# Kernel tuning notes

Measured on AMD Instinct MI355X. Metric: run time of the kernel, lower is better.

Reference implementation:

```python
import jax, jax.numpy as jnp
import numpy as np

B, N, D, C = 64, 512, 1024, 4  # batch, num_electrodes, d_model, num_classes
H = D // 2


def setup_inputs() -> dict:
    key = jax.random.key(0)
    ks = jax.random.split(key, 16)
    s = 0.02
    return {
        "Q": jax.random.normal(ks[0], (B, N, D), jnp.float32),
        "K": jax.random.normal(ks[1], (B, N, D), jnp.float32),
        "V": jax.random.normal(ks[2], (B, N, D), jnp.float32),
        "electrode_ids": jnp.arange(N, dtype=jnp.int64 if jax.config.jax_enable_x64 else jnp.int32),
        "emb": jax.random.normal(ks[3], (N, D), jnp.float32) * s,
        "dw1": jax.random.normal(ks[4], (H, D), jnp.float32) * s,
        "db1": jnp.zeros((H,), jnp.float32),
        "dw2": jax.random.normal(ks[5], (1, H), jnp.float32) * s,
        "db2": jnp.zeros((1,), jnp.float32),
        "sw1": jax.random.normal(ks[6], (H, D), jnp.float32) * s,
        "sb1": jnp.zeros((H,), jnp.float32),
        "sw2": jax.random.normal(ks[7], (1, H), jnp.float32) * s,
        "sb2": jnp.zeros((1,), jnp.float32),
        "dopamine_scale": jnp.asarray(1.0, jnp.float32),
        "serotonin_scale": jnp.asarray(1.0, jnp.float32),
        "fc_w": jax.random.normal(ks[8], (C, N * D), jnp.float32) * s,
        "fc_b": jnp.zeros((C,), jnp.float32),
    }


def reference(Q, K, V, electrode_ids, emb, dw1, db1, dw2, db2,
              sw1, sb1, sw2, sb2, dopamine_scale, serotonin_scale, fc_w, fc_b):
    e = emb[electrode_ids]                       # [N, D]
    Q = Q + e
    K = K + e
    V = V + e
    scale = jnp.sqrt(jnp.asarray(D, jnp.float32))
    scores = jnp.einsum('bnd,bmd->bnm', Q, K) / scale          # [B, N, N]
    probs = jax.nn.softmax(scores, axis=-1)
    entropy = -jnp.sum(probs * jnp.log(probs + 1e-6), axis=-1)  # [B, N]

    # dopamine MLP on Q tokens (eval mode -> dropout is identity)
    dh = jax.nn.relu(jnp.einsum('bnd,hd->bnh', Q, dw1) + db1)
    dopamine = jax.nn.sigmoid(jnp.einsum('bnh,oh->bno', dh, dw2) + db2)[..., 0]  # [B, N]

    # serotonin MLP on entropy broadcast to D identical features:
    # Linear(entropy * ones(D)) == entropy * W1.sum(axis=1) + b1 (same math, no [B,N,D] temp)
    sh = jax.nn.relu(entropy[..., None] * jnp.sum(sw1, axis=1) + sb1)            # [B, N, H]
    serotonin = jax.nn.sigmoid(jnp.einsum('bnh,oh->bno', sh, sw2) + sb2)[..., 0]  # [B, N]

    mod = dopamine_scale * dopamine[..., None] - serotonin_scale * serotonin[..., None]
    ms = scores + mod
    mu = jnp.mean(ms, axis=-1, keepdims=True)
    sd = jnp.std(ms, axis=-1, keepdims=True, ddof=1)  # torch.std default is unbiased
    ms = (ms - mu) / (sd + 1e-6)
    probs2 = jax.nn.softmax(ms, axis=-1)
    attn_out = jnp.einsum('bnm,bmd->bnd', probs2, V)   # [B, N, D]
    flat = attn_out.reshape(attn_out.shape[0], -1)      # [B, N*D]
    return flat @ fc_w.T + fc_b                          # [B, C]
```

## Files before the change

kernel.cpp:

```cpp
#include <hip/hip_runtime.h>

#define NN 512
#define ND 1024
#define NDW 524288
#define NBATCH 64

typedef __attribute__((ext_vector_type(8))) __bf16 bf16x8;
typedef __attribute__((ext_vector_type(4))) float f32x4;
typedef unsigned short u16;
typedef unsigned int u32;

__device__ __forceinline__ u16 f2bf(float x) {
    u32 u = __float_as_uint(x);
    u = (u + 0x7fffu + ((u >> 16) & 1u)) >> 16;
    return (u16)u;
}

__device__ __forceinline__ void dma16(const u16* g, const u16* l) {
    __builtin_amdgcn_global_load_lds(
        (const __attribute__((address_space(1))) u32*)(uintptr_t)g,
        (__attribute__((address_space(3))) u32*)(u32)(uintptr_t)l,
        16, 0, 0);
}

__global__ __launch_bounds__(256)
void prep_all(const float* __restrict__ Q, const float* __restrict__ K,
              const float* __restrict__ V, const int* __restrict__ eid,
              const float* __restrict__ emb,
              u16* __restrict__ Qe, u16* __restrict__ Ke, u16* __restrict__ VT,
              float* __restrict__ out, const float* __restrict__ fcb)
{
    __shared__ u16 T[64 * 72];
    const int bb = blockIdx.x;
    const int tid = threadIdx.x;

    if (bb < 16384) {
        size_t f = ((size_t)bb * 256 + tid) * 8;
        int n = (int)((f >> 10) & (NN - 1));
        int col = (int)(f & (ND - 1));
        const float* ep = emb + (size_t)eid[n] * ND + col;
        float4 e0 = *(const float4*)ep, e1 = *(const float4*)(ep + 4);
        {
            const float* qp = Q + f;
            float4 x0 = *(const float4*)qp, x1 = *(const float4*)(qp + 4);
            union { uint4 u; u16 s[8]; } o;
            o.s[0]=f2bf(x0.x+e0.x); o.s[1]=f2bf(x0.y+e0.y); o.s[2]=f2bf(x0.z+e0.z); o.s[3]=f2bf(x0.w+e0.w);
            o.s[4]=f2bf(x1.x+e1.x); o.s[5]=f2bf(x1.y+e1.y); o.s[6]=f2bf(x1.z+e1.z); o.s[7]=f2bf(x1.w+e1.w);
            *(uint4*)(Qe + f) = o.u;
        }
        {
            const float* kp = K + f;
            float4 x0 = *(const float4*)kp, x1 = *(const float4*)(kp + 4);
            union { uint4 u; u16 s[8]; } o;
            o.s[0]=f2bf(x0.x+e0.x); o.s[1]=f2bf(x0.y+e0.y); o.s[2]=f2bf(x0.z+e0.z); o.s[3]=f2bf(x0.w+e0.w);
            o.s[4]=f2bf(x1.x+e1.x); o.s[5]=f2bf(x1.y+e1.y); o.s[6]=f2bf(x1.z+e1.z); o.s[7]=f2bf(x1.w+e1.w);
            *(uint4*)(Ke + f) = o.u;
        }
    } else if (bb < 16384 + 8192) {
        const int t = bb - 16384;
        const int n0 = (t & 7) * 64, d0 = ((t >> 3) & 15) * 64, b = t >> 7;
        {
            const int r2 = (tid & 31) * 2;
            const int cg = tid >> 5;
            const int na = n0 + r2, nb = n0 + r2 + 1;
            const float* vp0 = V + ((size_t)b * NN + na) * ND + d0 + cg * 8;
            const float* vp1 = V + ((size_t)b * NN + nb) * ND + d0 + cg * 8;
            const float* ep0 = emb + (size_t)eid[na] * ND + d0 + cg * 8;
            const float* ep1 = emb + (size_t)eid[nb] * ND + d0 + cg * 8;
            float4 a0 = *(const float4*)vp0,       a1 = *(const float4*)(vp0 + 4);
            float4 b0 = *(const float4*)vp1,       b1 = *(const float4*)(vp1 + 4);
            float4 x0 = *(const float4*)ep0,       x1 = *(const float4*)(ep0 + 4);
            float4 y0 = *(const float4*)ep1,       y1 = *(const float4*)(ep1 + 4);
            float lo[8] = {a0.x+x0.x, a0.y+x0.y, a0.z+x0.z, a0.w+x0.w,
                           a1.x+x1.x, a1.y+x1.y, a1.z+x1.z, a1.w+x1.w};
            float hi[8] = {b0.x+y0.x, b0.y+y0.y, b0.z+y0.z, b0.w+y0.w,
                           b1.x+y1.x, b1.y+y1.y, b1.z+y1.z, b1.w+y1.w};
            #pragma unroll
            for (int j = 0; j < 8; ++j) {
                u32 pk = (u32)f2bf(lo[j]) | ((u32)f2bf(hi[j]) << 16);
                *(u32*)&T[(cg * 8 + j) * 72 + r2] = pk;
            }
        }
        __syncthreads();
        {
            const int dr = tid >> 2, ms = (tid & 3) * 16;
            u16* dst = VT + ((size_t)b * ND + d0 + dr) * NN + n0 + ms;
            *(uint4*)dst       = *(const uint4*)&T[dr * 72 + ms];
            *(uint4*)(dst + 8) = *(const uint4*)&T[dr * 72 + ms + 8];
        }
    } else {
        if (tid < NBATCH * 4) out[tid] = fcb[tid & 3];
    }
}

__global__ __launch_bounds__(512, 4)
void nma_attn(const u16* __restrict__ Qe, const u16* __restrict__ Ke,
              const u16* __restrict__ VT, const float* __restrict__ fcw,
              float* __restrict__ out)
{
    __shared__ __align__(16) u16 KV[NN * 32];
    __shared__ __align__(16) u16 Ps[32 * 520];
    __shared__ float red[8][32][4];
    __shared__ float rowM[32], rowInv[32], rowRden[32];

    const int tid  = threadIdx.x;
    const int w    = tid >> 6;
    const int lane = tid & 63;
    const int q    = lane >> 4;
    const int l15  = lane & 15;
    const int rr   = lane >> 2;
    const int seg  = lane & 3;
    const int bid  = blockIdx.x;
    const int jj   = bid >> 3;
    const int b    = (bid & 7) + ((jj >> 4) << 3);
    const int i0   = (jj & 15) * 32;
    const size_t bOff = (size_t)b * NN * ND;
    const int wrow = w * 64;

    const u16* aP0 = Qe + bOff + (size_t)(i0 + l15) * ND + q * 8;
    const u16* aP1 = aP0 + (size_t)16 * ND;
    const u16* KeB = Ke + bOff;
    const u16* VTB = VT + (size_t)b * ND * NN;

#define DMA_KE(KC) do {                                                         \
    _Pragma("unroll")                                                           \
    for (int ii_ = 0; ii_ < 4; ++ii_)                                           \
        dma16(KeB + (size_t)(wrow + ii_ * 16 + rr) * ND + (KC) * 32 + seg * 8,  \
              &KV[(wrow + ii_ * 16) * 32]);                                     \
    } while (0)

#define DMA_VT(H, MC) do {                                                      \
    _Pragma("unroll")                                                           \
    for (int ii_ = 0; ii_ < 4; ++ii_)                                           \
        dma16(VTB + (size_t)((H) * 512 + wrow + ii_ * 16 + rr) * NN             \
                  + (MC) * 32 + seg * 8,                                        \
              &KV[(wrow + ii_ * 16) * 32]);                                     \
    } while (0)

    f32x4 acc[2][4];
    #pragma unroll
    for (int it = 0; it < 2; ++it)
        #pragma unroll
        for (int mt = 0; mt < 4; ++mt)
            acc[it][mt] = (f32x4){0.f, 0.f, 0.f, 0.f};

    bf16x8 qc0, qc1, qn0, qn1;
    {
        qc0 = *(const bf16x8*)aP0;
        qc1 = *(const bf16x8*)aP1;
        DMA_KE(0);
    }

#define P2BODY(KC, C0, C1, N0, N1) do {                                         \
    asm volatile("s_waitcnt vmcnt(0)" ::: "memory");   \
    bf16x8 bfr[4];                                                              \
    _Pragma("unroll")                                                           \
    for (int mt = 0; mt < 4; ++mt)                                              \
        bfr[mt] = *(const bf16x8*)&KV[(wrow + mt * 16 + l15) * 32 + q * 8];     \
    asm volatile("s_waitcnt lgkmcnt(0)" ::: "memory");    \
    if ((KC) < 31) {                                                            \
        DMA_KE((KC) + 1);                    \
        N0 = *(const bf16x8*)(aP0 + ((KC) + 1) * 32);    \
        N1 = *(const bf16x8*)(aP1 + ((KC) + 1) * 32);                           \
    }                                                                           \
    _Pragma("unroll")                                                           \
    for (int mt = 0; mt < 4; ++mt) {                                            \
        acc[0][mt] = __builtin_amdgcn_mfma_f32_16x16x32_bf16(C0, bfr[mt], acc[0][mt], 0, 0, 0); \
        acc[1][mt] = __builtin_amdgcn_mfma_f32_16x16x32_bf16(C1, bfr[mt], acc[1][mt], 0, 0, 0); \
    } } while (0)

    for (int kc = 0; kc < 32; kc += 2) {
        P2BODY(kc,     qc0, qc1, qn0, qn1);
        P2BODY(kc + 1, qn0, qn1, qc0, qc1);
    }

    const float SC = 0.03125f;
    #pragma unroll
    for (int it = 0; it < 2; ++it)
        #pragma unroll
        for (int mt = 0; mt < 4; ++mt) {
            acc[it][mt][0] *= SC; acc[it][mt][1] *= SC;
            acc[it][mt][2] *= SC; acc[it][mt][3] *= SC;
        }
    float ssum[2][4], ssq[2][4], smax[2][4];
    #pragma unroll
    for (int it = 0; it < 2; ++it)
        #pragma unroll
        for (int r = 0; r < 4; ++r) {
            float s = 0.f, s2 = 0.f, mx = -3.4e38f;
            #pragma unroll
            for (int mt = 0; mt < 4; ++mt) {
                float v = acc[it][mt][r];
                s += v; s2 += v * v; mx = fmaxf(mx, v);
            }
            #pragma unroll
            for (int d = 1; d < 16; d <<= 1) {
                s  += __shfl_xor(s, d);
                s2 += __shfl_xor(s2, d);
                mx  = fmaxf(mx, __shfl_xor(mx, d));
            }
            ssum[it][r] = s; ssq[it][r] = s2; smax[it][r] = mx;
        }
    if (l15 == 0) {
        #pragma unroll
        for (int it = 0; it < 2; ++it)
            #pragma unroll
            for (int r = 0; r < 4; ++r) {
                int i = it * 16 + q * 4 + r;
                red[w][i][0] = ssum[it][r];
                red[w][i][1] = ssq[it][r];
                red[w][i][2] = smax[it][r];
            }
    }
    __syncthreads();
    if (tid < 32) {
        float s = 0.f, s2 = 0.f, mx = -3.4e38f;
        #pragma unroll
        for (int ww = 0; ww < 8; ++ww) {
            s  += red[ww][tid][0];
            s2 += red[ww][tid][1];
            mx  = fmaxf(mx, red[ww][tid][2]);
        }
        float mu  = s * (1.f / 512.f);
        float var = fmaxf((s2 - s * mu) * (1.f / 511.f), 0.f);
        float sd  = sqrtf(var);
        rowM[tid]   = mx;
        rowInv[tid] = 1.f / (sd + 1e-6f);
    }
    __syncthreads();
    float dsum[2][4];
    #pragma unroll
    for (int it = 0; it < 2; ++it)
        #pragma unroll
        for (int r = 0; r < 4; ++r) {
            int i = it * 16 + q * 4 + r;
            float M = rowM[i], inv = rowInv[i];
            float s = 0.f;
            #pragma unroll
            for (int mt = 0; mt < 4; ++mt) {
                float e = __expf((acc[it][mt][r] - M) * inv);
                acc[it][mt][r] = e; s += e;
            }
            #pragma unroll
            for (int d = 1; d < 16; d <<= 1) s += __shfl_xor(s, d);
            dsum[it][r] = s;
        }
    if (l15 == 0) {
        #pragma unroll
        for (int it = 0; it < 2; ++it)
            #pragma unroll
            for (int r = 0; r < 4; ++r)
                red[w][it * 16 + q * 4 + r][0] = dsum[it][r];
    }
    __syncthreads();
    if (tid < 32) {
        float s = 0.f;
        #pragma unroll
        for (int ww = 0; ww < 8; ++ww) s += red[ww][tid][0];
        rowRden[tid] = 1.f / s;
    }
    __syncthreads();
    #pragma unroll
    for (int it = 0; it < 2; ++it)
        #pragma unroll
        for (int r = 0; r < 4; ++r) {
            int i = it * 16 + q * 4 + r;
            float rd = rowRden[i];
            #pragma unroll
            for (int mt = 0; mt < 4; ++mt) {
                int m = wrow + mt * 16 + l15;
                Ps[i * 520 + m] = f2bf(acc[it][mt][r] * rd);
            }
        }
    __syncthreads();

    DMA_VT(0, 0);
    float fsum[4] = {0.f, 0.f, 0.f, 0.f};
    for (int h = 0; h < 2; ++h) {
        f32x4 oacc[2][4];
        #pragma unroll
        for (int it = 0; it < 2; ++it)
            #pragma unroll
            for (int dt = 0; dt < 4; ++dt)
                oacc[it][dt] = (f32x4){0.f, 0.f, 0.f, 0.f};
        for (int mc = 0; mc < 16; ++mc) {
            bf16x8 p0 = *(const bf16x8*)&Ps[l15 * 520 + mc * 32 + q * 8];
            bf16x8 p1 = *(const bf16x8*)&Ps[(16 + l15) * 520 + mc * 32 + q * 8];
            asm volatile("s_waitcnt vmcnt(0)" ::: "memory");
            bf16x8 bfr[4];
            #pragma unroll
            for (int dt = 0; dt < 4; ++dt)
                bfr[dt] = *(const bf16x8*)&KV[(wrow + dt * 16 + l15) * 32 + q * 8];
            asm volatile("s_waitcnt lgkmcnt(0)" ::: "memory");
            const int j = h * 16 + mc;
            if (j < 31) {
                const int jn = j + 1;
                DMA_VT(jn >> 4, jn & 15);
            }
            #pragma unroll
            for (int dt = 0; dt < 4; ++dt) {
                oacc[0][dt] = __builtin_amdgcn_mfma_f32_16x16x32_bf16(p0, bfr[dt], oacc[0][dt], 0, 0, 0);
                oacc[1][dt] = __builtin_amdgcn_mfma_f32_16x16x32_bf16(p1, bfr[dt], oacc[1][dt], 0, 0, 0);
            }
        }
        #pragma unroll
        for (int it = 0; it < 2; ++it) {
            #pragma unroll
            for (int r = 0; r < 4; ++r) {
                const int iglob = i0 + it * 16 + q * 4 + r;
                const float* fr = fcw + (size_t)iglob * ND + (h * 512 + wrow + l15);
                #pragma unroll
                for (int dt = 0; dt < 4; ++dt) {
                    const float o = oacc[it][dt][r];
                    fsum[0] += o * fr[dt * 16];
                    fsum[1] += o * fr[(size_t)NDW + dt * 16];
                    fsum[2] += o * fr[(size_t)2 * NDW + dt * 16];
                    fsum[3] += o * fr[(size_t)3 * NDW + dt * 16];
                }
            }
        }
    }
    #pragma unroll
    for (int c = 0; c < 4; ++c)
        #pragma unroll
        for (int d = 1; d < 64; d <<= 1)
            fsum[c] += __shfl_xor(fsum[c], d);
    if (lane == 0) {
        red[w][0][0] = fsum[0]; red[w][0][1] = fsum[1];
        red[w][0][2] = fsum[2]; red[w][0][3] = fsum[3];
    }
    __syncthreads();
    if (tid < 4) {
        float s = 0.f;
        #pragma unroll
        for (int ww = 0; ww < 8; ++ww) s += red[ww][0][tid];
        atomicAdd(&out[b * 4 + tid], s);
    }
#undef P2BODY
#undef DMA_KE
#undef DMA_VT
}

extern "C" void kernel_launch(void* const* d_in, const int* in_sizes, int n_in,
                              void* d_out, int out_size, void* d_ws, size_t ws_size,
                              hipStream_t stream) {
    (void)in_sizes; (void)n_in; (void)ws_size; (void)out_size;
    const float* Q   = (const float*)d_in[0];
    const float* K   = (const float*)d_in[1];
    const float* V   = (const float*)d_in[2];
    const int*   eid = (const int*)d_in[3];
    const float* emb = (const float*)d_in[4];
    const float* fcw = (const float*)d_in[15];
    const float* fcb = (const float*)d_in[16];
    float* out = (float*)d_out;

    u16* Qe = (u16*)d_ws;
    u16* Ke = Qe + (size_t)NBATCH * NN * ND;
    u16* VT = Ke + (size_t)NBATCH * NN * ND;

    prep_all<<<dim3(16384 + 8192 + 1), dim3(256), 0, stream>>>(
        Q, K, V, eid, emb, Qe, Ke, VT, out, fcb);
    nma_attn<<<dim3(1024), dim3(512), 0, stream>>>(Qe, Ke, VT, fcw, out);
}
```

Baseline: 655.3 us.

## Load K and V^T operands directly into registers instead of LDS DMA staging

Removes the shared-memory staging buffer that was filled by global_load_lds DMA, along with the explicit vmcnt/lgkmcnt waits. K and V^T MFMA operands are now read straight from global memory into registers and double-buffered across iterations. The goal is to cut LDS traffic, waits and shared memory footprint, which may allow more occupancy. In exchange it uses more registers, and the global loads are strided (16 rows by 16 bytes) with no cross-wave reuse through LDS.

```diff
diff --git a/kernel.cpp b/kernel.cpp
--- a/kernel.cpp
+++ b/kernel.cpp
@@ -14,13 +14,6 @@
     u32 u = __float_as_uint(x);
     u = (u + 0x7fffu + ((u >> 16) & 1u)) >> 16;
     return (u16)u;
-}
-
-__device__ __forceinline__ void dma16(const u16* g, const u16* l) {
-    __builtin_amdgcn_global_load_lds(
-        (const __attribute__((address_space(1))) u32*)(uintptr_t)g,
-        (__attribute__((address_space(3))) u32*)(u32)(uintptr_t)l,
-        16, 0, 0);
 }
 
 __global__ __launch_bounds__(256)
@@ -98,7 +91,6 @@
               const u16* __restrict__ VT, const float* __restrict__ fcw,
               float* __restrict__ out)
 {
-    __shared__ __align__(16) u16 KV[NN * 32];
     __shared__ __align__(16) u16 Ps[32 * 520];
     __shared__ float red[8][32][4];
     __shared__ float rowM[32], rowInv[32], rowRden[32];
@@ -108,8 +100,6 @@
     const int lane = tid & 63;
     const int q    = lane >> 4;
     const int l15  = lane & 15;
-    const int rr   = lane >> 2;
-    const int seg  = lane & 3;
     const int bid  = blockIdx.x;
     const int jj   = bid >> 3;
     const int b    = (bid & 7) + ((jj >> 4) << 3);
@@ -119,23 +109,8 @@
 
     const u16* aP0 = Qe + bOff + (size_t)(i0 + l15) * ND + q * 8;
     const u16* aP1 = aP0 + (size_t)16 * ND;
-    const u16* KeB = Ke + bOff;
-    const u16* VTB = VT + (size_t)b * ND * NN;
-
-#define DMA_KE(KC) do {                                                         \
-    _Pragma("unroll")                                                           \
-    for (int ii_ = 0; ii_ < 4; ++ii_)                                           \
-        dma16(KeB + (size_t)(wrow + ii_ * 16 + rr) * ND + (KC) * 32 + seg * 8,  \
-              &KV[(wrow + ii_ * 16) * 32]);                                     \
-    } while (0)
-
-#define DMA_VT(H, MC) do {                                                      \
-    _Pragma("unroll")                                                           \
-    for (int ii_ = 0; ii_ < 4; ++ii_)                                           \
-        dma16(VTB + (size_t)((H) * 512 + wrow + ii_ * 16 + rr) * NN             \
-                  + (MC) * 32 + seg * 8,                                        \
-              &KV[(wrow + ii_ * 16) * 32]);                                     \
-    } while (0)
+    const u16* bP  = Ke + bOff + (size_t)(wrow + l15) * ND + q * 8;
+    const u16* vP  = VT + (size_t)b * ND * NN + (size_t)(wrow + l15) * NN + q * 8;
 
     f32x4 acc[2][4];
     #pragma unroll
@@ -144,34 +119,30 @@
         for (int mt = 0; mt < 4; ++mt)
             acc[it][mt] = (f32x4){0.f, 0.f, 0.f, 0.f};
 
-    bf16x8 qc0, qc1, qn0, qn1;
-    {
-        qc0 = *(const bf16x8*)aP0;
-        qc1 = *(const bf16x8*)aP1;
-        DMA_KE(0);
-    }
-
-#define P2BODY(KC, C0, C1, N0, N1) do {                                         \
-    asm volatile("s_waitcnt vmcnt(0)" ::: "memory");   \
-    bf16x8 bfr[4];                                                              \
-    _Pragma("unroll")                                                           \
-    for (int mt = 0; mt < 4; ++mt)                                              \
-        bfr[mt] = *(const bf16x8*)&KV[(wrow + mt * 16 + l15) * 32 + q * 8];     \
-    asm volatile("s_waitcnt lgkmcnt(0)" ::: "memory");    \
+    bf16x8 qc0, qc1, qn0, qn1, bc[4], bn[4];
+    qc0 = *(const bf16x8*)aP0;
+    qc1 = *(const bf16x8*)aP1;
+    #pragma unroll
+    for (int mt = 0; mt < 4; ++mt)
+        bc[mt] = *(const bf16x8*)(bP + (size_t)(mt * 16) * ND);
+
+#define P2BODY(KC, C0, C1, BC, N0, N1, BN) do {                                 \
     if ((KC) < 31) {                                                            \
-        DMA_KE((KC) + 1);                    \
-        N0 = *(const bf16x8*)(aP0 + ((KC) + 1) * 32);    \
+        N0 = *(const bf16x8*)(aP0 + ((KC) + 1) * 32);                           \
         N1 = *(const bf16x8*)(aP1 + ((KC) + 1) * 32);                           \
+        _Pragma("unroll")                                                       \
+        for (int mt = 0; mt < 4; ++mt)                                          \
+            BN[mt] = *(const bf16x8*)(bP + (size_t)(mt * 16) * ND + ((KC) + 1) * 32); \
     }                                                                           \
     _Pragma("unroll")                                                           \
     for (int mt = 0; mt < 4; ++mt) {                                            \
-        acc[0][mt] = __builtin_amdgcn_mfma_f32_16x16x32_bf16(C0, bfr[mt], acc[0][mt], 0, 0, 0); \
-        acc[1][mt] = __builtin_amdgcn_mfma_f32_16x16x32_bf16(C1, bfr[mt], acc[1][mt], 0, 0, 0); \
+        acc[0][mt] = __builtin_amdgcn_mfma_f32_16x16x32_bf16(C0, BC[mt], acc[0][mt], 0, 0, 0); \
+        acc[1][mt] = __builtin_amdgcn_mfma_f32_16x16x32_bf16(C1, BC[mt], acc[1][mt], 0, 0, 0); \
     } } while (0)
 
     for (int kc = 0; kc < 32; kc += 2) {
-        P2BODY(kc,     qc0, qc1, qn0, qn1);
-        P2BODY(kc + 1, qn0, qn1, qc0, qc1);
+        P2BODY(kc,     qc0, qc1, bc, qn0, qn1, bn);
+        P2BODY(kc + 1, qn0, qn1, bn, qc0, qc1, bc);
     }
 
     const float SC = 0.03125f;
@@ -274,52 +245,68 @@
         }
     __syncthreads();
 
-    DMA_VT(0, 0);
     float fsum[4] = {0.f, 0.f, 0.f, 0.f};
-    for (int h = 0; h < 2; ++h) {
-        f32x4 oacc[2][4];
-        #pragma unroll
-        for (int it = 0; it < 2; ++it)
-            #pragma unroll
-            for (int dt = 0; dt < 4; ++dt)
-                oacc[it][dt] = (f32x4){0.f, 0.f, 0.f, 0.f};
-        for (int mc = 0; mc < 16; ++mc) {
-            bf16x8 p0 = *(const bf16x8*)&Ps[l15 * 520 + mc * 32 + q * 8];
-            bf16x8 p1 = *(const bf16x8*)&Ps[(16 + l15) * 520 + mc * 32 + q * 8];
-            asm volatile("s_waitcnt vmcnt(0)" ::: "memory");
-            bf16x8 bfr[4];
-            #pragma unroll
-            for (int dt = 0; dt < 4; ++dt)
-                bfr[dt] = *(const bf16x8*)&KV[(wrow + dt * 16 + l15) * 32 + q * 8];
-            asm volatile("s_waitcnt lgkmcnt(0)" ::: "memory");
-            const int j = h * 16 + mc;
-            if (j < 31) {
-                const int jn = j + 1;
-                DMA_VT(jn >> 4, jn & 15);
-            }
-            #pragma unroll
-            for (int dt = 0; dt < 4; ++dt) {
-                oacc[0][dt] = __builtin_amdgcn_mfma_f32_16x16x32_bf16(p0, bfr[dt], oacc[0][dt], 0, 0, 0);
-                oacc[1][dt] = __builtin_amdgcn_mfma_f32_16x16x32_bf16(p1, bfr[dt], oacc[1][dt], 0, 0, 0);
-            }
-        }
-        #pragma unroll
-        for (int it = 0; it < 2; ++it) {
-            #pragma unroll
-            for (int r = 0; r < 4; ++r) {
-                const int iglob = i0 + it * 16 + q * 4 + r;
-                const float* fr = fcw + (size_t)iglob * ND + (h * 512 + wrow + l15);
+    f32x4 oacc[2][4];
+    #pragma unroll
+    for (int it = 0; it < 2; ++it)
+        #pragma unroll
+        for (int dt = 0; dt < 4; ++dt)
+            oacc[it][dt] = (f32x4){0.f, 0.f, 0.f, 0.f};
+
+    bf16x8 vc[4], vn[4];
+    #pragma unroll
+    for (int dt = 0; dt < 4; ++dt)
+        vc[dt] = *(const bf16x8*)(vP + (size_t)(dt * 16) * NN);
+
+#define FCACC(H) do {                                                           \
+    _Pragma("unroll")                                                           \
+    for (int it = 0; it < 2; ++it) {                                            \
+        _Pragma("unroll")                                                       \
+        for (int r = 0; r < 4; ++r) {                                           \
+            const int iglob = i0 + it * 16 + q * 4 + r;                         \
+            const float* fr = fcw + (size_t)iglob * ND + ((H) * 512 + wrow + l15); \
+            _Pragma("unroll")                                                   \
+            for (int dt = 0; dt < 4; ++dt) {                                    \
+                const float o = oacc[it][dt][r];                                \
+                fsum[0] += o * fr[dt * 16];                                     \
+                fsum[1] += o * fr[(size_t)NDW + dt * 16];                       \
+                fsum[2] += o * fr[(size_t)2 * NDW + dt * 16];                   \
+                fsum[3] += o * fr[(size_t)3 * NDW + dt * 16];                   \
+            }                                                                   \
+        }                                                                       \
+    } } while (0)
+
+#define P4BODY(J, VC, VN) do {                                                  \
+    const int mc_ = (J) & 15;                                                   \
+    bf16x8 p0 = *(const bf16x8*)&Ps[l15 * 520 + mc_ * 32 + q * 8];              \
+    bf16x8 p1 = *(const bf16x8*)&Ps[(16 + l15) * 520 + mc_ * 32 + q * 8];       \
+    if ((J) < 31) {                                                             \
+        const int jn_ = (J) + 1;                                                \
+        const u16* vb_ = vP + (size_t)((jn_ >> 4) * 512) * NN + (jn_ & 15) * 32;\
+        _Pragma("unroll")                                                       \
+        for (int dt = 0; dt < 4; ++dt)                                          \
+            VN[dt] = *(const bf16x8*)(vb_ + (size_t)(dt * 16) * NN);            \
+    }                                                                           \
+    _Pragma("unroll")                                                           \
+    for (int dt = 0; dt < 4; ++dt) {                                            \
+        oacc[0][dt] = __builtin_amdgcn_mfma_f32_16x16x32_bf16(p0, VC[dt], oacc[0][dt], 0, 0, 0); \
+        oacc[1][dt] = __builtin_amdgcn_mfma_f32_16x16x32_bf16(p1, VC[dt], oacc[1][dt], 0, 0, 0); \
+    } } while (0)
+
+    for (int j = 0; j < 32; j += 2) {
+        if (j == 16) {
+            FCACC(0);
+            #pragma unroll
+            for (int it = 0; it < 2; ++it)
                 #pragma unroll
-                for (int dt = 0; dt < 4; ++dt) {
-                    const float o = oacc[it][dt][r];
-                    fsum[0] += o * fr[dt * 16];
-                    fsum[1] += o * fr[(size_t)NDW + dt * 16];
-                    fsum[2] += o * fr[(size_t)2 * NDW + dt * 16];
-                    fsum[3] += o * fr[(size_t)3 * NDW + dt * 16];
-                }
-            }
-        }
-    }
+                for (int dt = 0; dt < 4; ++dt)
+                    oacc[it][dt] = (f32x4){0.f, 0.f, 0.f, 0.f};
+        }
+        P4BODY(j,     vc, vn);
+        P4BODY(j + 1, vn, vc);
+    }
+    FCACC(1);
+
     #pragma unroll
     for (int c = 0; c < 4; ++c)
         #pragma unroll
@@ -337,8 +324,8 @@
         atomicAdd(&out[b * 4 + tid], s);
     }
 #undef P2BODY
-#undef DMA_KE
-#undef DMA_VT
+#undef P4BODY
+#undef FCACC
 }
 
 extern "C" void kernel_launch(void* const* d_in, const int* in_sizes, int n_in,
```

After: 777.5 us. 1.19x slower.
